# Kernel optimization log

Hardware: AMD Instinct MI355X
Metric: run time of the kernel (lower is better)

Reference implementation:

```python
import math
import jax, jax.numpy as jnp
import numpy as np

N_HEAD = 16

def setup_inputs() -> dict:
    key = jax.random.key(0)
    ks = jax.random.split(key, 6)
    B, T, C = 8, 2048, 1024
    x = jax.random.normal(ks[0], (B, T, C), dtype=jnp.float32)
    # Linear weights stored as (in, out); scaled ~ standard init
    W_attn = jax.random.normal(ks[1], (C, 3 * C), dtype=jnp.float32) * (1.0 / math.sqrt(C))
    b_attn = jnp.zeros((3 * C,), dtype=jnp.float32)
    W_proj = jax.random.normal(ks[2], (C, C), dtype=jnp.float32) * (1.0 / math.sqrt(C))
    b_proj = jnp.zeros((C,), dtype=jnp.float32)
    # E/F: torch.randn in the original; scale by 0.02 so softmax is non-degenerate
    E = jax.random.normal(ks[3], (N_HEAD, 128, T), dtype=jnp.float32) * 0.02
    F = jax.random.normal(ks[4], (N_HEAD, 128, T), dtype=jnp.float32) * 0.02
    return {"x": x, "W_attn": W_attn, "b_attn": b_attn,
            "W_proj": W_proj, "b_proj": b_proj, "E": E, "F": F}

def reference(x, W_attn, b_attn, W_proj, b_proj, E, F):
    B, T, C = x.shape
    H = N_HEAD
    D = C // H
    scale = 1.0 / math.sqrt(D)
    qkv = x @ W_attn + b_attn                       # [B,T,3C]
    q, k, v = jnp.split(qkv, 3, axis=-1)
    # [B,T,C] -> [B,H,T,D]
    q = q.reshape(B, T, H, D).transpose(0, 2, 1, 3)
    k = k.reshape(B, T, H, D).transpose(0, 2, 1, 3)
    v = v.reshape(B, T, H, D).transpose(0, 2, 1, 3)
    Et = E[:, :, :T]                                # [H,k,T]
    Ft = F[:, :, :T]
    k_proj = jnp.einsum('hkt,bhtd->bhkd', Et, k)    # [B,H,k,D]
    v_proj = jnp.einsum('hkt,bhtd->bhkd', Ft, v)
    att = jnp.einsum('bhtd,bhkd->bhtk', q, k_proj) * scale
    att = jax.nn.softmax(att, axis=-1)              # dropout p=0 -> identity
    y = jnp.einsum('bhtk,bhkd->bhtd', att, v_proj)
    y = y.transpose(0, 2, 1, 3).reshape(B, T, C)
    return y @ W_proj + b_proj
```

## Files before the change

### kernel.cpp

```cpp
#include <hip/hip_runtime.h>
#include <math.h>


constexpr int B_ = 8, T_ = 2048, C_ = 1024, H_ = 16, D_ = 64, KP = 128;
constexpr int M_ = B_ * T_;
constexpr int C3 = 3 * C_;
constexpr int K_ = C_;
constexpr int NT = K_ / 64;
constexpr int TCH = 4;

typedef __attribute__((ext_vector_type(8))) short bf16x8;
typedef __attribute__((ext_vector_type(4))) float f32x4;

__device__ __forceinline__ unsigned short f2bf(float f) {
  unsigned u = __builtin_bit_cast(unsigned, f);
  u += 0x7FFFu + ((u >> 16) & 1u);
  return (unsigned short)(u >> 16);
}
__device__ __forceinline__ float bf2f(unsigned short h) {
  unsigned u = ((unsigned)h) << 16;
  return __builtin_bit_cast(float, u);
}

#define GLOAD_LDS16(gptr, lptr)                                                \
  __builtin_amdgcn_global_load_lds(                                            \
      (const __attribute__((address_space(1))) void*)(gptr),                   \
      (__attribute__((address_space(3))) void*)(lptr), 16, 0, 0)

__global__ __launch_bounds__(256) void cast_bf16(
    const float* __restrict__ in, unsigned short* __restrict__ hi, int n4)
{
  int i = blockIdx.x * 256 + threadIdx.x;
  if (i >= n4) return;
  const float4 v = reinterpret_cast<const float4*>(in)[i];
  ushort4 h;
  h.x = f2bf(v.x); h.y = f2bf(v.y); h.z = f2bf(v.z); h.w = f2bf(v.w);
  reinterpret_cast<ushort4*>(hi)[i] = h;
}

__global__ __launch_bounds__(256) void cast_tr(
    const float* __restrict__ W, unsigned short* __restrict__ Tb,
    int rows, int cols)
{
  __shared__ float tile[32][33];
  const int c0 = blockIdx.x * 32, r0 = blockIdx.y * 32;
  const int tx = threadIdx.x & 31, ty = threadIdx.x >> 5;
  #pragma unroll
  for (int i = 0; i < 4; ++i)
    tile[ty + i * 8][tx] = W[(size_t)(r0 + ty + i * 8) * cols + c0 + tx];
  __syncthreads();
  #pragma unroll
  for (int i = 0; i < 4; ++i) {
    const int cr = ty + i * 8;
    Tb[(size_t)(c0 + cr) * rows + r0 + tx] = f2bf(tile[tx][cr]);
  }
}

template <bool BFOUT>
__global__ __launch_bounds__(512, 2) void gemm256(
    const unsigned short* __restrict__ A, const unsigned short* __restrict__ BT,
    const float* __restrict__ bias, float* __restrict__ Cf,
    unsigned short* __restrict__ Cb, int ldc)
{
  __shared__ __attribute__((aligned(16))) char lds[131072];

  const int tid  = threadIdx.x;
  const int lane = tid & 63;
  const int w    = tid >> 6;
  const int wr   = w >> 2;
  const int wc   = w & 3;
  const int col  = lane & 15;
  const int quad = lane >> 4;

  const int ntx = ldc >> 8;
  int wg = blockIdx.x;
  wg = (wg & 7) * (gridDim.x >> 3) + (wg >> 3);
  const int bx = wg % ntx, by = wg / ntx;
  const int m0 = by << 8, n0 = bx << 8;

  const int kq   = quad * 8;
  const int rowL = w * 16 + col;
  const int mOff = (rowL >> 6) * 128 + (rowL & 63);
  const int nOff = (rowL >> 5) * 64 + (rowL & 31);
  const int dstO = w * 2048 + lane * 16;

#define STAGE_A(H, KT0, BUFSEL)                                                \
  { const int kb_ = (KT0) * 64 + kq;                                           \
    _Pragma("unroll")                                                          \
    for (int l = 0; l < 2; ++l)                                                \
      GLOAD_LDS16(A + (size_t)(m0 + mOff + (H) * 64) * K_ + kb_ + l * 32,      \
                  lds + (BUFSEL) * 65536 + (H) * 16384 + dstO + l * 1024); }

#define STAGE_B(H, KT0, BUFSEL)                                                \
  { const int kb_ = (KT0) * 64 + kq;                                           \
    _Pragma("unroll")                                                          \
    for (int l = 0; l < 2; ++l)                                                \
      GLOAD_LDS16(BT + (size_t)(n0 + nOff + (H) * 32) * K_ + kb_ + l * 32,     \
                  lds + (BUFSEL) * 65536 + 32768 + (H) * 16384 + dstO +        \
                      l * 1024); }

  const int laneB = lane * 16;
  const int aB0 = wr * 8192 + laneB;
  const int aB1 = 16384 + aB0;
  const int bB0 = 32768 + wc * 4096 + laneB;
  const int bB1 = 16384 + bB0;

  f32x4 acc[8][4];
  #pragma unroll
  for (int a = 0; a < 8; ++a)
    #pragma unroll
    for (int c = 0; c < 4; ++c)
      acc[a][c] = (f32x4){0.f, 0.f, 0.f, 0.f};

  bf16x8 av[4][2], b0v[2][2], b1v[2][2];

#define MFMA_Q(QM, QN, BV)                                                     \
  __builtin_amdgcn_s_setprio(1);                                               \
  _Pragma("unroll")                                                            \
  for (int j = 0; j < 2; ++j)                                                  \
    _Pragma("unroll")                                                          \
    for (int ks = 0; ks < 2; ++ks)                                             \
      _Pragma("unroll")                                                        \
      for (int i = 0; i < 4; ++i)                                              \
        acc[(QM) * 4 + i][(QN) * 2 + j] =                                      \
            __builtin_amdgcn_mfma_f32_16x16x32_bf16(                           \
                av[i][ks], BV[j][ks], acc[(QM) * 4 + i][(QN) * 2 + j], 0, 0, 0);\
  __builtin_amdgcn_s_setprio(0);

  STAGE_A(0, 0, 0);
  STAGE_B(0, 0, 0);
  STAGE_B(1, 0, 0);
  STAGE_A(1, 0, 0);
  asm volatile("s_waitcnt vmcnt(4)" ::: "memory");
  STAGE_A(0, 1, 1);
  STAGE_B(0, 1, 1);
  STAGE_B(1, 1, 1);
  asm volatile("s_waitcnt vmcnt(6)" ::: "memory");
  __builtin_amdgcn_s_barrier();

#define TILE(KT, CUR)                                                          \
  {                                                                            \
    const char* cb = lds + (CUR) * 65536;                                      \
                       \
    _Pragma("unroll")                                                          \
    for (int i = 0; i < 4; ++i)                                                \
      _Pragma("unroll")                                                        \
      for (int ks = 0; ks < 2; ++ks)                                           \
        av[i][ks] = *reinterpret_cast<const bf16x8*>(                          \
            cb + aB0 + i * 2048 + ks * 1024);                                  \
    _Pragma("unroll")                                                          \
    for (int j = 0; j < 2; ++j)                                                \
      _Pragma("unroll")                                                        \
      for (int ks = 0; ks < 2; ++ks)                                           \
        b0v[j][ks] = *reinterpret_cast<const bf16x8*>(                         \
            cb + bB0 + j * 2048 + ks * 1024);                                  \
    if ((KT) + 1 < NT) { STAGE_A(1, (KT) + 1, (CUR) ^ 1); }                    \
    asm volatile("s_waitcnt lgkmcnt(8)" ::: "memory");                         \
    __builtin_amdgcn_s_barrier();                                              \
    asm volatile("s_waitcnt lgkmcnt(0)" ::: "memory");                         \
    __builtin_amdgcn_sched_barrier(0);                                         \
    MFMA_Q(0, 0, b0v);                                                         \
    __builtin_amdgcn_s_barrier();                                              \
                        \
    _Pragma("unroll")                                                          \
    for (int j = 0; j < 2; ++j)                                                \
      _Pragma("unroll")                                                        \
      for (int ks = 0; ks < 2; ++ks)                                           \
        b1v[j][ks] = *reinterpret_cast<const bf16x8*>(                         \
            cb + bB1 + j * 2048 + ks * 1024);                                  \
    if ((KT) + 2 < NT) { STAGE_A(0, (KT) + 2, (CUR)); }                        \
    __builtin_amdgcn_s_barrier();                                              \
    asm volatile("s_waitcnt lgkmcnt(0)" ::: "memory");                         \
    __builtin_amdgcn_sched_barrier(0);                                         \
    MFMA_Q(0, 1, b1v);                                                         \
    __builtin_amdgcn_s_barrier();                                              \
                        \
    _Pragma("unroll")                                                          \
    for (int i = 0; i < 4; ++i)                                                \
      _Pragma("unroll")                                                        \
      for (int ks = 0; ks < 2; ++ks)                                           \
        av[i][ks] = *reinterpret_cast<const bf16x8*>(                          \
            cb + aB1 + i * 2048 + ks * 1024);                                  \
    if ((KT) + 2 < NT) { STAGE_B(0, (KT) + 2, (CUR)); }                        \
    __builtin_amdgcn_s_barrier();                                              \
    asm volatile("s_waitcnt lgkmcnt(0)" ::: "memory");                         \
    __builtin_amdgcn_sched_barrier(0);                                         \
    MFMA_Q(1, 1, b1v);                                                         \
    __builtin_amdgcn_s_barrier();                                              \
        \
    if ((KT) + 2 < NT) { STAGE_B(1, (KT) + 2, (CUR)); }                        \
    __builtin_amdgcn_s_barrier();                                              \
    __builtin_amdgcn_sched_barrier(0);                                         \
    MFMA_Q(1, 0, b0v);                                                         \
    if ((KT) < NT - 2) {                                                       \
      asm volatile("s_waitcnt vmcnt(6)" ::: "memory");                         \
    } else if ((KT) == NT - 2) {                                               \
      asm volatile("s_waitcnt vmcnt(0)" ::: "memory");                         \
    }                                                                          \
    __builtin_amdgcn_s_barrier();                                              \
  }

  for (int kt = 0; kt < NT; kt += 2) {
    TILE(kt, 0);
    TILE(kt + 1, 1);
  }
#undef TILE
#undef MFMA_Q
#undef STAGE_A
#undef STAGE_B

  #pragma unroll
  for (int a = 0; a < 8; ++a) {
    const int r = m0 + wr * 128 + (a >> 2) * 64 + (a & 3) * 16 + quad * 4;
    #pragma unroll
    for (int c = 0; c < 4; ++c) {
      const int cc = n0 + wc * 64 + (c >> 1) * 32 + (c & 1) * 16 + col;
      const float bv = bias[cc];
      #pragma unroll
      for (int rg = 0; rg < 4; ++rg) {
        const float v = acc[a][c][rg] + bv;
        const size_t o = (size_t)(r + rg) * ldc + cc;
        if constexpr (BFOUT) Cb[o] = f2bf(v);
        else Cf[o] = v;
      }
    }
  }
}

__global__ __launch_bounds__(256) void proj_mfma(
    const unsigned short* __restrict__ Eh, const unsigned short* __restrict__ kb,
    int ldk, float* __restrict__ part)
{
  __shared__ unsigned short sE[KP * 72];
  __shared__ unsigned short sK[D_ * 72];

  const int bh = blockIdx.x;
  const int tc = blockIdx.y;
  const int b = bh >> 4, h = bh & 15;
  const int tid = threadIdx.x;
  const int lane = tid & 63;
  const int w = tid >> 6;
  const int col = lane & 15;
  const int quad = lane >> 4;
  const int tq = tid >> 4;
  const int dq = tid & 15;

  f32x4 acc[2][4];
  #pragma unroll
  for (int i = 0; i < 2; ++i)
    #pragma unroll
    for (int j = 0; j < 4; ++j) acc[i][j] = (f32x4){0.f, 0.f, 0.f, 0.f};

  for (int s = 0; s < 8; ++s) {
    const int t0 = tc * 512 + s * 64;
    #pragma unroll
    for (int l = 0; l < 4; ++l) {
      const int idx = l * 256 + tid;
      const int kk = idx >> 3, seg = idx & 7;
      *reinterpret_cast<uint4*>(sE + kk * 72 + seg * 8) =
          *reinterpret_cast<const uint4*>(
              Eh + (size_t)(h * KP + kk) * T_ + t0 + seg * 8);
    }
    {
      const size_t gbase = (size_t)(b * T_ + t0 + tq * 4) * ldk + h * D_ + dq * 4;
      ushort4 r[4];
      #pragma unroll
      for (int rr = 0; rr < 4; ++rr)
        r[rr] = *reinterpret_cast<const ushort4*>(kb + gbase + (size_t)rr * ldk);
      #pragma unroll
      for (int c = 0; c < 4; ++c) {
        ushort4 t;
        t.x = (&r[0].x)[c]; t.y = (&r[1].x)[c];
        t.z = (&r[2].x)[c]; t.w = (&r[3].x)[c];
        *reinterpret_cast<ushort4*>(sK + (dq * 4 + c) * 72 + tq * 4) = t;
      }
    }
    __syncthreads();

    bf16x8 av[2][2];
    #pragma unroll
    for (int i = 0; i < 2; ++i)
      #pragma unroll
      for (int ks = 0; ks < 2; ++ks)
        av[i][ks] = *reinterpret_cast<const bf16x8*>(
            sE + ((w * 2 + i) * 16 + col) * 72 + ks * 32 + quad * 8);
    #pragma unroll
    for (int j = 0; j < 4; ++j)
      #pragma unroll
      for (int ks = 0; ks < 2; ++ks) {
        const bf16x8 bv = *reinterpret_cast<const bf16x8*>(
            sK + (j * 16 + col) * 72 + ks * 32 + quad * 8);
        #pragma unroll
        for (int i = 0; i < 2; ++i)
          acc[i][j] = __builtin_amdgcn_mfma_f32_16x16x32_bf16(av[i][ks], bv, acc[i][j], 0, 0, 0);
      }
    __syncthreads();
  }

  float* op = part + ((size_t)bh * TCH + tc) * (KP * D_);
  #pragma unroll
  for (int i = 0; i < 2; ++i) {
    const int kkb = w * 32 + i * 16 + quad * 4;
    #pragma unroll
    for (int j = 0; j < 4; ++j) {
      const int d = j * 16 + col;
      #pragma unroll
      for (int rg = 0; rg < 4; ++rg)
        op[(kkb + rg) * D_ + d] = acc[i][j][rg];
    }
  }
}

__global__ __launch_bounds__(256) void reduce_k(
    const float* __restrict__ part, unsigned short* __restrict__ kprojh)
{
  const int idx = blockIdx.x * 256 + threadIdx.x;
  const int bh = idx >> 13;
  const int i = idx & 8191;
  float s = 0.f;
  #pragma unroll
  for (int c = 0; c < TCH; ++c)
    s += part[((size_t)bh * TCH + c) * 8192 + i];
  kprojh[idx] = f2bf(s);
}

__global__ __launch_bounds__(256) void reduce_v(
    const float* __restrict__ part, unsigned short* __restrict__ vpTh)
{
  __shared__ float sums[KP * 66];
  const int bh = blockIdx.x;
  const int tid = threadIdx.x;
  #pragma unroll
  for (int j = 0; j < 32; ++j) {
    const int i = j * 256 + tid;
    float s = 0.f;
    #pragma unroll
    for (int c = 0; c < TCH; ++c)
      s += part[((size_t)bh * TCH + c) * 8192 + i];
    sums[(i >> 6) * 66 + (i & 63)] = s;
  }
  __syncthreads();
  #pragma unroll
  for (int j = 0; j < 32; ++j) {
    const int i = j * 256 + tid;
    vpTh[(size_t)bh * 8192 + i] = f2bf(sums[(i & 127) * 66 + (i >> 7)]);
  }
}

__global__ __launch_bounds__(256) void attn_mfma(
    const unsigned short* __restrict__ qkv, const unsigned short* __restrict__ kprojh,
    const unsigned short* __restrict__ vpTh, unsigned short* __restrict__ yh)
{
  __shared__ __attribute__((aligned(16))) char lds[35072];
  unsigned short* Qh = (unsigned short*)(lds);
  unsigned short* Kp = (unsigned short*)(lds + 9216);
  unsigned short* Vh = (unsigned short*)(lds);
  unsigned short* Ps = (unsigned short*)(lds + 17408);
  float* atts = (float*)(lds + 34816);

  const int tid  = threadIdx.x;
  const int lane = tid & 63;
  const int w    = tid >> 6;
  const int col  = lane & 15;
  const int quad = lane >> 4;
  const int bh = blockIdx.x >> 5;
  const int tch = blockIdx.x & 31;
  const int b = bh >> 4, h = bh & 15;
  const int t0 = tch * 64;

  {
    const unsigned short* qg = qkv + (size_t)(b * T_ + t0) * C3 + h * D_;
    #pragma unroll
    for (int l = 0; l < 4; ++l) {
      const int idx = l * 256 + tid;
      const int t = idx >> 4, dc = (idx & 15) << 2;
      *reinterpret_cast<ushort4*>(Qh + t * 72 + dc) =
          *reinterpret_cast<const ushort4*>(qg + (size_t)t * C3 + dc);
    }
    const unsigned short* kg = kprojh + (size_t)bh * 8192;
    #pragma unroll
    for (int l = 0; l < 8; ++l) {
      const int idx = l * 256 + tid;
      const int kk = idx >> 4, dc = (idx & 15) << 2;
      *reinterpret_cast<ushort4*>(Kp + kk * 72 + dc) =
          *reinterpret_cast<const ushort4*>(kg + kk * 64 + dc);
    }
  }
  __syncthreads();

  f32x4 s[8];
  #pragma unroll
  for (int i = 0; i < 8; ++i) s[i] = (f32x4){0.f, 0.f, 0.f, 0.f};
  bf16x8 bq[2];
  #pragma unroll
  for (int ks = 0; ks < 2; ++ks)
    bq[ks] = *reinterpret_cast<const bf16x8*>(
        Qh + (w * 16 + col) * 72 + ks * 32 + quad * 8);
  #pragma unroll
  for (int i = 0; i < 8; ++i)
    #pragma unroll
    for (int ks = 0; ks < 2; ++ks) {
      const bf16x8 a = *reinterpret_cast<const bf16x8*>(
          Kp + (i * 16 + col) * 72 + ks * 32 + quad * 8);
      s[i] = __builtin_amdgcn_mfma_f32_16x16x32_bf16(a, bq[ks], s[i], 0, 0, 0);
    }

  float mx = -3.0e38f;
  #pragma unroll
  for (int i = 0; i < 8; ++i)
    #pragma unroll
    for (int rg = 0; rg < 4; ++rg) {
      s[i][rg] *= 0.125f;
      mx = fmaxf(mx, s[i][rg]);
    }
  mx = fmaxf(mx, __shfl_xor(mx, 16));
  mx = fmaxf(mx, __shfl_xor(mx, 32));
  float sum = 0.f;
  #pragma unroll
  for (int i = 0; i < 8; ++i)
    #pragma unroll
    for (int rg = 0; rg < 4; ++rg) {
      const float e = __expf(s[i][rg] - mx);
      s[i][rg] = e;
      sum += e;
    }
  sum += __shfl_xor(sum, 16);
  sum += __shfl_xor(sum, 32);
  const float inv = 1.f / sum;
  __syncthreads();

  {
    const unsigned short* vg = vpTh + (size_t)bh * 8192;
    #pragma unroll
    for (int l = 0; l < 8; ++l) {
      const int idx = l * 256 + tid;
      const int d = idx >> 5, kc = (idx & 31) << 2;
      *reinterpret_cast<ushort4*>(Vh + d * 136 + kc) =
          *reinterpret_cast<const ushort4*>(vg + d * 128 + kc);
    }
  }
  #pragma unroll
  for (int i = 0; i < 8; ++i) {
    ushort4 hp;
    hp.x = f2bf(s[i][0]); hp.y = f2bf(s[i][1]);
    hp.z = f2bf(s[i][2]); hp.w = f2bf(s[i][3]);
    *reinterpret_cast<ushort4*>(Ps + (w * 16 + col) * 136 + i * 16 + quad * 4) = hp;
  }
  if (quad == 0) atts[w * 16 + col] = inv;
  __syncthreads();

  f32x4 y[4];
  #pragma unroll
  for (int j = 0; j < 4; ++j) y[j] = (f32x4){0.f, 0.f, 0.f, 0.f};
  bf16x8 ap[4];
  #pragma unroll
  for (int ks = 0; ks < 4; ++ks)
    ap[ks] = *reinterpret_cast<const bf16x8*>(
        Ps + (w * 16 + col) * 136 + ks * 32 + quad * 8);
  #pragma unroll
  for (int j = 0; j < 4; ++j)
    #pragma unroll
    for (int ks = 0; ks < 4; ++ks) {
      const bf16x8 bv = *reinterpret_cast<const bf16x8*>(
          Vh + (j * 16 + col) * 136 + ks * 32 + quad * 8);
      y[j] = __builtin_amdgcn_mfma_f32_16x16x32_bf16(ap[ks], bv, y[j], 0, 0, 0);
    }

  const f32x4 inv4 = *reinterpret_cast<const f32x4*>(atts + w * 16 + quad * 4);
  #pragma unroll
  for (int j = 0; j < 4; ++j)
    #pragma unroll
    for (int rg = 0; rg < 4; ++rg) {
      const int t = t0 + w * 16 + quad * 4 + rg;
      const int d = j * 16 + col;
      yh[(size_t)(b * T_ + t) * C_ + h * D_ + d] = f2bf(y[j][rg] * inv4[rg]);
    }
}

extern "C" void kernel_launch(void* const* d_in, const int* in_sizes, int n_in,
                              void* d_out, int out_size, void* d_ws, size_t ws_size,
                              hipStream_t stream) {
  (void)in_sizes; (void)n_in; (void)out_size; (void)ws_size;
  const float* x      = (const float*)d_in[0];
  const float* W_attn = (const float*)d_in[1];
  const float* b_attn = (const float*)d_in[2];
  const float* W_proj = (const float*)d_in[3];
  const float* b_proj = (const float*)d_in[4];
  const float* E      = (const float*)d_in[5];
  const float* F      = (const float*)d_in[6];
  float* out = (float*)d_out;

  unsigned short* xh   = (unsigned short*)d_ws;
  unsigned short* qkvh = xh + (size_t)M_ * C_;
  unsigned short* WaT  = qkvh + (size_t)M_ * C3;
  unsigned short* WpT  = WaT + (size_t)C3 * C_;
  unsigned short* Eh   = WpT + (size_t)C_ * C_;
  unsigned short* Fh   = Eh + (size_t)H_ * KP * T_;
  float* part = (float*)(Fh + (size_t)H_ * KP * T_);
  unsigned short* kprojh = (unsigned short*)(part + (size_t)B_ * H_ * TCH * KP * D_);
  unsigned short* vpTh   = kprojh + (size_t)B_ * H_ * KP * D_;
  unsigned short* yh = xh;

  cast_bf16<<<(M_ * C_ / 4 + 255) / 256, 256, 0, stream>>>(x, xh, M_ * C_ / 4);
  cast_bf16<<<(H_ * KP * T_ / 4 + 255) / 256, 256, 0, stream>>>(E, Eh, H_ * KP * T_ / 4);
  cast_bf16<<<(H_ * KP * T_ / 4 + 255) / 256, 256, 0, stream>>>(F, Fh, H_ * KP * T_ / 4);
  cast_tr<<<dim3(C3 / 32, C_ / 32), 256, 0, stream>>>(W_attn, WaT, C_, C3);
  cast_tr<<<dim3(C_ / 32, C_ / 32), 256, 0, stream>>>(W_proj, WpT, C_, C_);

  gemm256<true><<<dim3((M_ / 256) * (C3 / 256)), 512, 0, stream>>>(
      xh, WaT, b_attn, nullptr, qkvh, C3);

  proj_mfma<<<dim3(B_ * H_, TCH), 256, 0, stream>>>(Eh, qkvh + C_, C3, part);
  reduce_k<<<(B_ * H_ * KP * D_) / 256, 256, 0, stream>>>(part, kprojh);

  proj_mfma<<<dim3(B_ * H_, TCH), 256, 0, stream>>>(Fh, qkvh + 2 * C_, C3, part);
  reduce_v<<<B_ * H_, 256, 0, stream>>>(part, vpTh);

  attn_mfma<<<B_ * H_ * (T_ / 64), 256, 0, stream>>>(qkvh, kprojh, vpTh, yh);

  gemm256<false><<<dim3((M_ / 256) * (C_ / 256)), 512, 0, stream>>>(
      yh, WpT, b_proj, out, nullptr, C_);
}
```

Before: 384.5 us.

## Merge cast kernels, drop split-K reductions, and loop attention over multiple tiles

Merges the three elementwise casts into one launch and the two weight transposes into another. The projection kernels now split the output rows across blocks instead of splitting T, so each block runs the full T loop and writes bf16 directly; the partial buffers and reduce kernels are gone. The attention kernel loads K_proj and V_proj into LDS once per block and loops over four 64-row query tiles, reading Q straight from global memory. This cuts launch count, intermediate traffic and redundant LDS loads, at the cost of far fewer blocks for the projection stage (256 instead of 512, each with a longer serial loop) and larger LDS use in attention.

```diff
diff --git a/kernel.cpp b/kernel.cpp
--- a/kernel.cpp
+++ b/kernel.cpp
@@ -7,7 +7,6 @@
 constexpr int C3 = 3 * C_;
 constexpr int K_ = C_;
 constexpr int NT = K_ / 64;
-constexpr int TCH = 4;
 
 typedef __attribute__((ext_vector_type(8))) short bf16x8;
 typedef __attribute__((ext_vector_type(4))) float f32x4;
@@ -17,33 +16,43 @@
   u += 0x7FFFu + ((u >> 16) & 1u);
   return (unsigned short)(u >> 16);
 }
-__device__ __forceinline__ float bf2f(unsigned short h) {
-  unsigned u = ((unsigned)h) << 16;
-  return __builtin_bit_cast(float, u);
-}
 
 #define GLOAD_LDS16(gptr, lptr)                                                \
   __builtin_amdgcn_global_load_lds(                                            \
       (const __attribute__((address_space(1))) void*)(gptr),                   \
       (__attribute__((address_space(3))) void*)(lptr), 16, 0, 0)
 
-__global__ __launch_bounds__(256) void cast_bf16(
-    const float* __restrict__ in, unsigned short* __restrict__ hi, int n4)
+__global__ __launch_bounds__(256) void cast3(
+    const float* __restrict__ x, const float* __restrict__ E,
+    const float* __restrict__ F, unsigned short* __restrict__ xh,
+    unsigned short* __restrict__ Eh, unsigned short* __restrict__ Fh)
 {
-  int i = blockIdx.x * 256 + threadIdx.x;
-  if (i >= n4) return;
-  const float4 v = reinterpret_cast<const float4*>(in)[i];
+  constexpr int n4x = M_ * C_ / 4;
+  constexpr int n4e = H_ * KP * T_ / 4;
+  const int i = blockIdx.x * 256 + threadIdx.x;
+  const float* src; unsigned short* dst; int j;
+  if (i < n4x)            { src = x; dst = xh; j = i; }
+  else if (i < n4x + n4e) { src = E; dst = Eh; j = i - n4x; }
+  else                    { src = F; dst = Fh; j = i - n4x - n4e; }
+  const float4 v = reinterpret_cast<const float4*>(src)[j];
   ushort4 h;
   h.x = f2bf(v.x); h.y = f2bf(v.y); h.z = f2bf(v.z); h.w = f2bf(v.w);
-  reinterpret_cast<ushort4*>(hi)[i] = h;
-}
-
-__global__ __launch_bounds__(256) void cast_tr(
-    const float* __restrict__ W, unsigned short* __restrict__ Tb,
-    int rows, int cols)
+  reinterpret_cast<ushort4*>(dst)[j] = h;
+}
+
+__global__ __launch_bounds__(256) void cast_tr2(
+    const float* __restrict__ Wa, unsigned short* __restrict__ WaT,
+    const float* __restrict__ Wp, unsigned short* __restrict__ WpT)
 {
   __shared__ float tile[32][33];
-  const int c0 = blockIdx.x * 32, r0 = blockIdx.y * 32;
+  const float* W; unsigned short* Tb; int bx, by, rows, cols;
+  const int flat = blockIdx.x;
+  if (flat < 3072) { W = Wa; Tb = WaT; bx = flat % 96; by = flat / 96;
+                     rows = C_; cols = C3; }
+  else             { const int f2 = flat - 3072;
+                     W = Wp; Tb = WpT; bx = f2 % 32; by = f2 / 32;
+                     rows = C_; cols = C_; }
+  const int c0 = bx * 32, r0 = by * 32;
   const int tx = threadIdx.x & 31, ty = threadIdx.x >> 5;
   #pragma unroll
   for (int i = 0; i < 4; ++i)
@@ -227,15 +236,16 @@
   }
 }
 
-__global__ __launch_bounds__(256) void proj_mfma(
+template <bool TRANS>
+__global__ __launch_bounds__(256) void proj_full(
     const unsigned short* __restrict__ Eh, const unsigned short* __restrict__ kb,
-    int ldk, float* __restrict__ part)
+    unsigned short* __restrict__ outp)
 {
-  __shared__ unsigned short sE[KP * 72];
+  __shared__ unsigned short sE[64 * 72];
   __shared__ unsigned short sK[D_ * 72];
 
   const int bh = blockIdx.x;
-  const int tc = blockIdx.y;
+  const int kh = blockIdx.y;
   const int b = bh >> 4, h = bh & 15;
   const int tid = threadIdx.x;
   const int lane = tid & 63;
@@ -245,28 +255,26 @@
   const int tq = tid >> 4;
   const int dq = tid & 15;
 
-  f32x4 acc[2][4];
+  f32x4 acc[4];
   #pragma unroll
-  for (int i = 0; i < 2; ++i)
-    #pragma unroll
-    for (int j = 0; j < 4; ++j) acc[i][j] = (f32x4){0.f, 0.f, 0.f, 0.f};
-
-  for (int s = 0; s < 8; ++s) {
-    const int t0 = tc * 512 + s * 64;
-    #pragma unroll
-    for (int l = 0; l < 4; ++l) {
+  for (int j = 0; j < 4; ++j) acc[j] = (f32x4){0.f, 0.f, 0.f, 0.f};
+
+  for (int s = 0; s < 32; ++s) {
+    const int t0 = s * 64;
+    #pragma unroll
+    for (int l = 0; l < 2; ++l) {
       const int idx = l * 256 + tid;
       const int kk = idx >> 3, seg = idx & 7;
       *reinterpret_cast<uint4*>(sE + kk * 72 + seg * 8) =
           *reinterpret_cast<const uint4*>(
-              Eh + (size_t)(h * KP + kk) * T_ + t0 + seg * 8);
+              Eh + (size_t)(h * KP + kh * 64 + kk) * T_ + t0 + seg * 8);
     }
     {
-      const size_t gbase = (size_t)(b * T_ + t0 + tq * 4) * ldk + h * D_ + dq * 4;
+      const size_t gbase = (size_t)(b * T_ + t0 + tq * 4) * C3 + h * D_ + dq * 4;
       ushort4 r[4];
       #pragma unroll
       for (int rr = 0; rr < 4; ++rr)
-        r[rr] = *reinterpret_cast<const ushort4*>(kb + gbase + (size_t)rr * ldk);
+        r[rr] = *reinterpret_cast<const ushort4*>(kb + gbase + (size_t)rr * C3);
       #pragma unroll
       for (int c = 0; c < 4; ++c) {
         ushort4 t;
@@ -277,106 +285,65 @@
     }
     __syncthreads();
 
-    bf16x8 av[2][2];
-    #pragma unroll
-    for (int i = 0; i < 2; ++i)
-      #pragma unroll
-      for (int ks = 0; ks < 2; ++ks)
-        av[i][ks] = *reinterpret_cast<const bf16x8*>(
-            sE + ((w * 2 + i) * 16 + col) * 72 + ks * 32 + quad * 8);
+    bf16x8 av[2];
+    #pragma unroll
+    for (int ks = 0; ks < 2; ++ks)
+      av[ks] = *reinterpret_cast<const bf16x8*>(
+          sE + (w * 16 + col) * 72 + ks * 32 + quad * 8);
     #pragma unroll
     for (int j = 0; j < 4; ++j)
       #pragma unroll
       for (int ks = 0; ks < 2; ++ks) {
         const bf16x8 bv = *reinterpret_cast<const bf16x8*>(
             sK + (j * 16 + col) * 72 + ks * 32 + quad * 8);
-        #pragma unroll
-        for (int i = 0; i < 2; ++i)
-          acc[i][j] = __builtin_amdgcn_mfma_f32_16x16x32_bf16(av[i][ks], bv, acc[i][j], 0, 0, 0);
+        acc[j] = __builtin_amdgcn_mfma_f32_16x16x32_bf16(av[ks], bv, acc[j], 0, 0, 0);
       }
     __syncthreads();
   }
 
-  float* op = part + ((size_t)bh * TCH + tc) * (KP * D_);
-  #pragma unroll
-  for (int i = 0; i < 2; ++i) {
-    const int kkb = w * 32 + i * 16 + quad * 4;
+  const int kkb = kh * 64 + w * 16 + quad * 4;
+  if constexpr (!TRANS) {
+    unsigned short* op = outp + (size_t)bh * 8192;
     #pragma unroll
     for (int j = 0; j < 4; ++j) {
       const int d = j * 16 + col;
       #pragma unroll
       for (int rg = 0; rg < 4; ++rg)
-        op[(kkb + rg) * D_ + d] = acc[i][j][rg];
-    }
-  }
-}
-
-__global__ __launch_bounds__(256) void reduce_k(
-    const float* __restrict__ part, unsigned short* __restrict__ kprojh)
-{
-  const int idx = blockIdx.x * 256 + threadIdx.x;
-  const int bh = idx >> 13;
-  const int i = idx & 8191;
-  float s = 0.f;
-  #pragma unroll
-  for (int c = 0; c < TCH; ++c)
-    s += part[((size_t)bh * TCH + c) * 8192 + i];
-  kprojh[idx] = f2bf(s);
-}
-
-__global__ __launch_bounds__(256) void reduce_v(
-    const float* __restrict__ part, unsigned short* __restrict__ vpTh)
-{
-  __shared__ float sums[KP * 66];
-  const int bh = blockIdx.x;
-  const int tid = threadIdx.x;
-  #pragma unroll
-  for (int j = 0; j < 32; ++j) {
-    const int i = j * 256 + tid;
-    float s = 0.f;
-    #pragma unroll
-    for (int c = 0; c < TCH; ++c)
-      s += part[((size_t)bh * TCH + c) * 8192 + i];
-    sums[(i >> 6) * 66 + (i & 63)] = s;
-  }
-  __syncthreads();
-  #pragma unroll
-  for (int j = 0; j < 32; ++j) {
-    const int i = j * 256 + tid;
-    vpTh[(size_t)bh * 8192 + i] = f2bf(sums[(i & 127) * 66 + (i >> 7)]);
-  }
-}
-
-__global__ __launch_bounds__(256) void attn_mfma(
+        op[(kkb + rg) * D_ + d] = f2bf(acc[j][rg]);
+    }
+  } else {
+    unsigned short* op = outp + (size_t)bh * 8192;
+    #pragma unroll
+    for (int j = 0; j < 4; ++j) {
+      const int d = j * 16 + col;
+      ushort4 hp;
+      hp.x = f2bf(acc[j][0]); hp.y = f2bf(acc[j][1]);
+      hp.z = f2bf(acc[j][2]); hp.w = f2bf(acc[j][3]);
+      *reinterpret_cast<ushort4*>(op + d * KP + kkb) = hp;
+    }
+  }
+}
+
+__global__ __launch_bounds__(256) void attn2(
     const unsigned short* __restrict__ qkv, const unsigned short* __restrict__ kprojh,
     const unsigned short* __restrict__ vpTh, unsigned short* __restrict__ yh)
 {
-  __shared__ __attribute__((aligned(16))) char lds[35072];
-  unsigned short* Qh = (unsigned short*)(lds);
-  unsigned short* Kp = (unsigned short*)(lds + 9216);
-  unsigned short* Vh = (unsigned short*)(lds);
-  unsigned short* Ps = (unsigned short*)(lds + 17408);
-  float* atts = (float*)(lds + 34816);
+  __shared__ __attribute__((aligned(16))) char lds[53248];
+  unsigned short* Kp = (unsigned short*)(lds);
+  unsigned short* Vh = (unsigned short*)(lds + 18432);
+  unsigned short* Ps = (unsigned short*)(lds + 35840);
 
   const int tid  = threadIdx.x;
   const int lane = tid & 63;
   const int w    = tid >> 6;
   const int col  = lane & 15;
   const int quad = lane >> 4;
-  const int bh = blockIdx.x >> 5;
-  const int tch = blockIdx.x & 31;
+  const int bh   = blockIdx.x >> 3;
+  const int tcb  = blockIdx.x & 7;
   const int b = bh >> 4, h = bh & 15;
-  const int t0 = tch * 64;
+  const int tBase = tcb * 256;
 
   {
-    const unsigned short* qg = qkv + (size_t)(b * T_ + t0) * C3 + h * D_;
-    #pragma unroll
-    for (int l = 0; l < 4; ++l) {
-      const int idx = l * 256 + tid;
-      const int t = idx >> 4, dc = (idx & 15) << 2;
-      *reinterpret_cast<ushort4*>(Qh + t * 72 + dc) =
-          *reinterpret_cast<const ushort4*>(qg + (size_t)t * C3 + dc);
-    }
     const unsigned short* kg = kprojh + (size_t)bh * 8192;
     #pragma unroll
     for (int l = 0; l < 8; ++l) {
@@ -385,51 +352,6 @@
       *reinterpret_cast<ushort4*>(Kp + kk * 72 + dc) =
           *reinterpret_cast<const ushort4*>(kg + kk * 64 + dc);
     }
-  }
-  __syncthreads();
-
-  f32x4 s[8];
-  #pragma unroll
-  for (int i = 0; i < 8; ++i) s[i] = (f32x4){0.f, 0.f, 0.f, 0.f};
-  bf16x8 bq[2];
-  #pragma unroll
-  for (int ks = 0; ks < 2; ++ks)
-    bq[ks] = *reinterpret_cast<const bf16x8*>(
-        Qh + (w * 16 + col) * 72 + ks * 32 + quad * 8);
-  #pragma unroll
-  for (int i = 0; i < 8; ++i)
-    #pragma unroll
-    for (int ks = 0; ks < 2; ++ks) {
-      const bf16x8 a = *reinterpret_cast<const bf16x8*>(
-          Kp + (i * 16 + col) * 72 + ks * 32 + quad * 8);
-      s[i] = __builtin_amdgcn_mfma_f32_16x16x32_bf16(a, bq[ks], s[i], 0, 0, 0);
-    }
-
-  float mx = -3.0e38f;
-  #pragma unroll
-  for (int i = 0; i < 8; ++i)
-    #pragma unroll
-    for (int rg = 0; rg < 4; ++rg) {
-      s[i][rg] *= 0.125f;
-      mx = fmaxf(mx, s[i][rg]);
-    }
-  mx = fmaxf(mx, __shfl_xor(mx, 16));
-  mx = fmaxf(mx, __shfl_xor(mx, 32));
-  float sum = 0.f;
-  #pragma unroll
-  for (int i = 0; i < 8; ++i)
-    #pragma unroll
-    for (int rg = 0; rg < 4; ++rg) {
-      const float e = __expf(s[i][rg] - mx);
-      s[i][rg] = e;
-      sum += e;
-    }
-  sum += __shfl_xor(sum, 16);
-  sum += __shfl_xor(sum, 32);
-  const float inv = 1.f / sum;
-  __syncthreads();
-
-  {
     const unsigned short* vg = vpTh + (size_t)bh * 8192;
     #pragma unroll
     for (int l = 0; l < 8; ++l) {
@@ -439,42 +361,87 @@
           *reinterpret_cast<const ushort4*>(vg + d * 128 + kc);
     }
   }
-  #pragma unroll
-  for (int i = 0; i < 8; ++i) {
-    ushort4 hp;
-    hp.x = f2bf(s[i][0]); hp.y = f2bf(s[i][1]);
-    hp.z = f2bf(s[i][2]); hp.w = f2bf(s[i][3]);
-    *reinterpret_cast<ushort4*>(Ps + (w * 16 + col) * 136 + i * 16 + quad * 4) = hp;
-  }
-  if (quad == 0) atts[w * 16 + col] = inv;
   __syncthreads();
 
-  f32x4 y[4];
-  #pragma unroll
-  for (int j = 0; j < 4; ++j) y[j] = (f32x4){0.f, 0.f, 0.f, 0.f};
-  bf16x8 ap[4];
-  #pragma unroll
-  for (int ks = 0; ks < 4; ++ks)
-    ap[ks] = *reinterpret_cast<const bf16x8*>(
-        Ps + (w * 16 + col) * 136 + ks * 32 + quad * 8);
-  #pragma unroll
-  for (int j = 0; j < 4; ++j)
-    #pragma unroll
-    for (int ks = 0; ks < 4; ++ks) {
-      const bf16x8 bv = *reinterpret_cast<const bf16x8*>(
-          Vh + (j * 16 + col) * 136 + ks * 32 + quad * 8);
-      y[j] = __builtin_amdgcn_mfma_f32_16x16x32_bf16(ap[ks], bv, y[j], 0, 0, 0);
-    }
-
-  const f32x4 inv4 = *reinterpret_cast<const f32x4*>(atts + w * 16 + quad * 4);
-  #pragma unroll
-  for (int j = 0; j < 4; ++j)
-    #pragma unroll
-    for (int rg = 0; rg < 4; ++rg) {
-      const int t = t0 + w * 16 + quad * 4 + rg;
-      const int d = j * 16 + col;
-      yh[(size_t)(b * T_ + t) * C_ + h * D_ + d] = f2bf(y[j][rg] * inv4[rg]);
-    }
+  for (int tc = 0; tc < 4; ++tc) {
+    const int t0 = tBase + tc * 64;
+
+    const unsigned short* qg =
+        qkv + (size_t)(b * T_ + t0 + w * 16 + col) * C3 + h * D_;
+    bf16x8 bq[2];
+    #pragma unroll
+    for (int ks = 0; ks < 2; ++ks)
+      bq[ks] = *reinterpret_cast<const bf16x8*>(qg + ks * 32 + quad * 8);
+
+    f32x4 s[8];
+    #pragma unroll
+    for (int i = 0; i < 8; ++i) s[i] = (f32x4){0.f, 0.f, 0.f, 0.f};
+    #pragma unroll
+    for (int i = 0; i < 8; ++i)
+      #pragma unroll
+      for (int ks = 0; ks < 2; ++ks) {
+        const bf16x8 a = *reinterpret_cast<const bf16x8*>(
+            Kp + (i * 16 + col) * 72 + ks * 32 + quad * 8);
+        s[i] = __builtin_amdgcn_mfma_f32_16x16x32_bf16(a, bq[ks], s[i], 0, 0, 0);
+      }
+
+    float mx = -3.0e38f;
+    #pragma unroll
+    for (int i = 0; i < 8; ++i)
+      #pragma unroll
+      for (int rg = 0; rg < 4; ++rg) {
+        s[i][rg] *= 0.125f;
+        mx = fmaxf(mx, s[i][rg]);
+      }
+    mx = fmaxf(mx, __shfl_xor(mx, 16));
+    mx = fmaxf(mx, __shfl_xor(mx, 32));
+    float sum = 0.f;
+    #pragma unroll
+    for (int i = 0; i < 8; ++i)
+      #pragma unroll
+      for (int rg = 0; rg < 4; ++rg) {
+        const float e = __expf(s[i][rg] - mx);
+        s[i][rg] = e;
+        sum += e;
+      }
+    sum += __shfl_xor(sum, 16);
+    sum += __shfl_xor(sum, 32);
+    const float inv = 1.f / sum;
+
+    #pragma unroll
+    for (int i = 0; i < 8; ++i) {
+      ushort4 hp;
+      hp.x = f2bf(s[i][0] * inv); hp.y = f2bf(s[i][1] * inv);
+      hp.z = f2bf(s[i][2] * inv); hp.w = f2bf(s[i][3] * inv);
+      *reinterpret_cast<ushort4*>(Ps + (w * 16 + col) * 136 + i * 16 + quad * 4) = hp;
+    }
+
+    f32x4 y[4];
+    #pragma unroll
+    for (int j = 0; j < 4; ++j) y[j] = (f32x4){0.f, 0.f, 0.f, 0.f};
+    bf16x8 ap[4];
+    #pragma unroll
+    for (int ks = 0; ks < 4; ++ks)
+      ap[ks] = *reinterpret_cast<const bf16x8*>(
+          Ps + (w * 16 + col) * 136 + ks * 32 + quad * 8);
+    #pragma unroll
+    for (int j = 0; j < 4; ++j)
+      #pragma unroll
+      for (int ks = 0; ks < 4; ++ks) {
+        const bf16x8 bv = *reinterpret_cast<const bf16x8*>(
+            Vh + (j * 16 + col) * 136 + ks * 32 + quad * 8);
+        y[j] = __builtin_amdgcn_mfma_f32_16x16x32_bf16(ap[ks], bv, y[j], 0, 0, 0);
+      }
+
+    #pragma unroll
+    for (int j = 0; j < 4; ++j)
+      #pragma unroll
+      for (int rg = 0; rg < 4; ++rg) {
+        const int t = t0 + w * 16 + quad * 4 + rg;
+        const int d = j * 16 + col;
+        yh[(size_t)(b * T_ + t) * C_ + h * D_ + d] = f2bf(y[j][rg]);
+      }
+  }
 }
 
 extern "C" void kernel_launch(void* const* d_in, const int* in_sizes, int n_in,
@@ -496,27 +463,22 @@
   unsigned short* WpT  = WaT + (size_t)C3 * C_;
   unsigned short* Eh   = WpT + (size_t)C_ * C_;
   unsigned short* Fh   = Eh + (size_t)H_ * KP * T_;
-  float* part = (float*)(Fh + (size_t)H_ * KP * T_);
-  unsigned short* kprojh = (unsigned short*)(part + (size_t)B_ * H_ * TCH * KP * D_);
+  unsigned short* kprojh = Fh + (size_t)H_ * KP * T_;
   unsigned short* vpTh   = kprojh + (size_t)B_ * H_ * KP * D_;
   unsigned short* yh = xh;
 
-  cast_bf16<<<(M_ * C_ / 4 + 255) / 256, 256, 0, stream>>>(x, xh, M_ * C_ / 4);
-  cast_bf16<<<(H_ * KP * T_ / 4 + 255) / 256, 256, 0, stream>>>(E, Eh, H_ * KP * T_ / 4);
-  cast_bf16<<<(H_ * KP * T_ / 4 + 255) / 256, 256, 0, stream>>>(F, Fh, H_ * KP * T_ / 4);
-  cast_tr<<<dim3(C3 / 32, C_ / 32), 256, 0, stream>>>(W_attn, WaT, C_, C3);
-  cast_tr<<<dim3(C_ / 32, C_ / 32), 256, 0, stream>>>(W_proj, WpT, C_, C_);
+  cast3<<<(M_ * C_ / 4 + 2 * (H_ * KP * T_ / 4)) / 256, 256, 0, stream>>>(
+      x, E, F, xh, Eh, Fh);
+  cast_tr2<<<3072 + 1024, 256, 0, stream>>>(W_attn, WaT, W_proj, WpT);
 
   gemm256<true><<<dim3((M_ / 256) * (C3 / 256)), 512, 0, stream>>>(
       xh, WaT, b_attn, nullptr, qkvh, C3);
 
-  proj_mfma<<<dim3(B_ * H_, TCH), 256, 0, stream>>>(Eh, qkvh + C_, C3, part);
-  reduce_k<<<(B_ * H_ * KP * D_) / 256, 256, 0, stream>>>(part, kprojh);
-
-  proj_mfma<<<dim3(B_ * H_, TCH), 256, 0, stream>>>(Fh, qkvh + 2 * C_, C3, part);
-  reduce_v<<<B_ * H_, 256, 0, stream>>>(part, vpTh);
-
-  attn_mfma<<<B_ * H_ * (T_ / 64), 256, 0, stream>>>(qkvh, kprojh, vpTh, yh);
+  proj_full<false><<<dim3(B_ * H_, 2), 256, 0, stream>>>(Eh, qkvh + C_, kprojh);
+
+  proj_full<true><<<dim3(B_ * H_, 2), 256, 0, stream>>>(Fh, qkvh + 2 * C_, vpTh);
+
+  attn2<<<B_ * H_ * (T_ / 256), 256, 0, stream>>>(qkvh, kprojh, vpTh, yh);
 
   gemm256<false><<<dim3((M_ / 256) * (C_ / 256)), 512, 0, stream>>>(
       yh, WpT, b_proj, out, nullptr, C_);
```

New measurement: 396.9 us. +3.2%, slower.
